# Kernel tuning notes

Measured on AMD Instinct MI355X. Metric: run time of the kernel, lower is better.

The kernel has to match this reference:

```python
import jax, jax.numpy as jnp
import numpy as np

B_BLK = 64      # sparse_block_size
LOCAL = 4       # sparse_local_num_blocks
GLOB = 2        # sparse_global_num_blocks
STRIDE = 4      # sparse_global_block_stride
NH = 16
NKV = 4
HD = 128
SCALE = HD ** -0.5
NEG = -1e9


def _build_block_index(num_blocks):
    """Static per-query-block key-block index table + validity mask."""
    max_sel = LOCAL + 1 + GLOB
    idx = np.zeros((num_blocks, max_sel), np.int32)
    valid = np.zeros((num_blocks, max_sel), bool)
    for t in range(num_blocks):
        local = list(range(max(0, t - LOCAL), t + 1))
        cand = list(range(0, t + 1, max(1, STRIDE)))
        glob = cand[-GLOB:] if (GLOB > 0 and len(cand) > 0) else []
        sel = sorted(set(local + glob))
        idx[t, :len(sel)] = sel
        valid[t, :len(sel)] = True
    return idx, valid


def _rotate_half(x):
    x1, x2 = jnp.split(x, 2, axis=-1)
    return jnp.concatenate((-x2, x1), axis=-1)


def setup_inputs() -> dict:
    key = jax.random.key(0)
    ks = jax.random.split(key, 7)
    bsz, S, H = 1, 4096, 2048
    return {
        "hidden_states": jax.random.normal(ks[0], (bsz, S, H), jnp.float32) * 0.02,
        "cos": jax.random.uniform(ks[1], (bsz, S, HD), jnp.float32, -1.0, 1.0),
        "sin": jax.random.uniform(ks[2], (bsz, S, HD), jnp.float32, -1.0, 1.0),
        "wq": jax.random.normal(ks[3], (NH * HD, H), jnp.float32) * 0.02,
        "wk": jax.random.normal(ks[4], (NKV * HD, H), jnp.float32) * 0.02,
        "wv": jax.random.normal(ks[5], (NKV * HD, H), jnp.float32) * 0.02,
        "wo": jax.random.normal(ks[6], (H, NH * HD), jnp.float32) * 0.02,
    }


def reference(hidden_states, cos, sin, wq, wk, wv, wo):
    b, S, H = hidden_states.shape
    # QKV projections (nn.Linear: x @ W.T), split heads -> [b, h, S, d]
    q = (hidden_states @ wq.T).reshape(b, S, NH, HD).transpose(0, 2, 1, 3)
    k = (hidden_states @ wk.T).reshape(b, S, NKV, HD).transpose(0, 2, 1, 3)
    v = (hidden_states @ wv.T).reshape(b, S, NKV, HD).transpose(0, 2, 1, 3)
    # RoPE (cos/sin broadcast over heads)
    c = cos[:, None, :, :]
    s = sin[:, None, :, :]
    q = q * c + _rotate_half(q) * s
    k = k * c + _rotate_half(k) * s
    # GQA: repeat KV heads
    n_rep = NH // NKV
    k = jnp.repeat(k, n_rep, axis=1)
    v = jnp.repeat(v, n_rep, axis=1)
    # Block-sparse local+global attention (S divisible by B_BLK -> no padding)
    T = S // B_BLK
    q_blk = q.reshape(b, NH, T, B_BLK, HD)
    k_blk = k.reshape(b, NH, T, B_BLK, HD)
    v_blk = v.reshape(b, NH, T, B_BLK, HD)
    idx, valid = _build_block_index(T)           # [T, Smax] static
    Smax = idx.shape[1]
    k_sel = k_blk[:, :, idx]                     # [b,h,T,Smax,Bk,d]
    v_sel = v_blk[:, :, idx]
    scores = jnp.einsum('bhtqd,bhtspd->bhtqsp', q_blk, k_sel) * SCALE
    # causal intra-block mask on the diagonal block, -inf on padded slots
    intra = jnp.triu(jnp.full((B_BLK, B_BLK), NEG, jnp.float32), 1)
    is_diag = jnp.asarray(idx == np.arange(T)[:, None], jnp.float32)  # [T,Smax]
    mask = is_diag[:, None, :, None] * intra[None, :, None, :]        # [T,Bq,Smax,Bk]
    mask = mask + jnp.where(jnp.asarray(valid)[:, None, :, None], 0.0, NEG)
    scores = scores + mask[None, None]
    scores = scores.reshape(b, NH, T, B_BLK, Smax * B_BLK)
    probs = jax.nn.softmax(scores, axis=-1)
    out = jnp.einsum('bhtqk,bhtkd->bhtqd', probs,
                     v_sel.reshape(b, NH, T, Smax * B_BLK, HD))
    out = out.reshape(b, NH, S, HD).transpose(0, 2, 1, 3).reshape(b, S, NH * HD)
    return out @ wo.T
```

## Files before the change

### kernel.cpp

```cpp
#include <hip/hip_runtime.h>

typedef unsigned short u16;
typedef short bf16x8 __attribute__((ext_vector_type(8)));
typedef float f32x4 __attribute__((ext_vector_type(4)));

#define S_LEN 4096
#define NHEADS 16
#define NKVH 4
#define HDIM 128
#define HID 2048
#define NQKV 3072

__device__ __forceinline__ u16 f2bf(float x) {
  union { float f; unsigned u; } v; v.f = x;
  unsigned r = v.u + 0x7fffu + ((v.u >> 16) & 1u);
  return (u16)(r >> 16);
}
__device__ __forceinline__ float bf2f(u16 x) {
  union { unsigned u; float f; } v; v.u = ((unsigned)x) << 16;
  return v.f;
}
__device__ __forceinline__ void async16(u16* lds, const u16* g) {
  __builtin_amdgcn_global_load_lds((const __attribute__((address_space(1))) void*)g,
                                   (__attribute__((address_space(3))) void*)lds, 16, 0, 0);
}

__global__ __launch_bounds__(256) void cast_f32_bf16(const float* __restrict__ in,
                                                     u16* __restrict__ out, int n4) {
  int i = blockIdx.x * 256 + threadIdx.x;
  if (i >= n4) return;
  float4 v = ((const float4*)in)[i];
  ushort4 o;
  o.x = f2bf(v.x); o.y = f2bf(v.y); o.z = f2bf(v.z); o.w = f2bf(v.w);
  ((ushort4*)out)[i] = o;
}

#define VMC4 asm volatile("s_waitcnt vmcnt(4)" ::: "memory")
#define VMC0 asm volatile("s_waitcnt vmcnt(0)" ::: "memory")
#define NOVM ((void)0)

#define STAGE_A(buf, h, kt) do { \
    async16(&As[buf][adst[h][0]], asrc[h][0] + (size_t)(kt) * 64); \
    async16(&As[buf][adst[h][1]], asrc[h][1] + (size_t)(kt) * 64); \
  } while (0)
#define STAGE_B(buf, h, kt) do { \
    async16(&Bs[buf][bdst[h][0]], bsrc[h][0] + (size_t)(kt) * 64); \
    async16(&Bs[buf][bdst[h][1]], bsrc[h][1] + (size_t)(kt) * 64); \
  } while (0)

#define RD_A(cur, mh) do { \
    _Pragma("unroll") \
    for (int i_ = 0; i_ < 4; ++i_) { \
      const int m64_ = (wm * 128 + ((mh) * 4 + i_) * 16 + l16) * 64; \
      af[i_][0] = *(const bf16x8*)&As[cur][m64_ + ((quad ^ x7) * 8)]; \
      af[i_][1] = *(const bf16x8*)&As[cur][m64_ + (((4 + quad) ^ x7) * 8)]; \
    } } while (0)

#define RD_B(cur, nh, dst) do { \
    _Pragma("unroll") \
    for (int j_ = 0; j_ < 2; ++j_) { \
      const int n64_ = (wn * 64 + ((nh) * 2 + j_) * 16 + l16) * 64; \
      dst[j_][0] = *(const bf16x8*)&Bs[cur][n64_ + ((quad ^ x7) * 8)]; \
      dst[j_][1] = *(const bf16x8*)&Bs[cur][n64_ + (((4 + quad) ^ x7) * 8)]; \
    } } while (0)

#define PH(READS, STAGE_STMT, MH, NH, BSET, VM) do { \
    READS; \
    STAGE_STMT; \
    __builtin_amdgcn_s_barrier(); \
    asm volatile("s_waitcnt lgkmcnt(0)" ::: "memory"); \
    __builtin_amdgcn_sched_barrier(0); \
    __builtin_amdgcn_s_setprio(1); \
    _Pragma("unroll") \
    for (int ks_ = 0; ks_ < 2; ++ks_) \
      _Pragma("unroll") \
      for (int i_ = 0; i_ < 4; ++i_) \
        _Pragma("unroll") \
        for (int j_ = 0; j_ < 2; ++j_) \
          acc[(MH) * 4 + i_][(NH) * 2 + j_] = __builtin_amdgcn_mfma_f32_16x16x32_bf16( \
              af[i_][ks_], BSET[j_][ks_], acc[(MH) * 4 + i_][(NH) * 2 + j_], 0, 0, 0); \
    __builtin_amdgcn_s_setprio(0); \
    VM; \
    __builtin_amdgcn_s_barrier(); \
  } while (0)

template<bool OUT_BF16>
__global__ __launch_bounds__(512, 2) void gemm8p(const u16* __restrict__ A, const u16* __restrict__ B,
                                                 void* __restrict__ Cp, int M, int N, int K) {
  __shared__ __align__(16) u16 As[2][256 * 64];
  __shared__ __align__(16) u16 Bs[2][256 * 64];
  const int tid = threadIdx.x;
  const int w = tid >> 6, l = tid & 63, quad = l >> 4, l16 = l & 15;
  const int wm = w >> 2, wn = w & 3;
  const int x7 = l16 & 7;
  const int bm = blockIdx.x, bn = blockIdx.y;

  const u16* asrc[2][2]; int adst[2][2];
  const u16* bsrc[2][2]; int bdst[2][2];
#pragma unroll
  for (int h = 0; h < 2; ++h)
#pragma unroll
    for (int j = 0; j < 2; ++j) {
      int u = j * 512 + w * 64 + l;
      int r = u >> 3, cc = u & 7;
      int ma = ((r >> 6) << 7) + (h << 6) + (r & 63);
      asrc[h][j] = A + (size_t)(bm * 256 + ma) * K + (size_t)((cc ^ (ma & 7)) * 8);
      int nb = ((r >> 5) << 6) + (h << 5) + (r & 31);
      bsrc[h][j] = B + (size_t)(bn * 256 + nb) * K + (size_t)((cc ^ (nb & 7)) * 8);
      int r0 = j * 64 + w * 8;
      adst[h][j] = (((r0 >> 6) << 7) + (h << 6) + (r0 & 63)) * 64;
      bdst[h][j] = (((r0 >> 5) << 6) + (h << 5) + (r0 & 31)) * 64;
    }

  f32x4 acc[8][4];
#pragma unroll
  for (int i = 0; i < 8; ++i)
#pragma unroll
    for (int j = 0; j < 4; ++j) acc[i][j] = f32x4{0.f, 0.f, 0.f, 0.f};

  bf16x8 af[4][2], b0f[2][2], b1f[2][2];

  STAGE_A(0, 0, 0); STAGE_B(0, 0, 0); STAGE_B(0, 1, 0); STAGE_A(0, 1, 0);
  STAGE_A(1, 0, 1); STAGE_B(1, 0, 1);
  VMC4;
  __builtin_amdgcn_s_barrier();

  const int NI = K >> 7;
  for (int it = 0; it < NI; ++it) {
    const int t1 = 2 * it + 1, t2 = 2 * it + 2, t3 = 2 * it + 3;
    const bool full = (it + 1 < NI);
    PH(RD_A(0, 0); RD_B(0, 0, b0f), STAGE_B(1, 1, t1),            0, 0, b0f, NOVM);
    PH(RD_B(0, 1, b1f),             STAGE_A(1, 1, t1),            0, 1, b1f, NOVM);
    PH(RD_A(0, 1),                  if (full) STAGE_A(0, 0, t2),  1, 1, b1f, NOVM);
    PH(((void)0),                   if (full) STAGE_B(0, 0, t2),  1, 0, b0f, if (full) VMC4; else VMC0);
    PH(RD_A(1, 0); RD_B(1, 0, b0f), if (full) STAGE_B(0, 1, t2),  0, 0, b0f, NOVM);
    PH(RD_B(1, 1, b1f),             if (full) STAGE_A(0, 1, t2),  0, 1, b1f, NOVM);
    PH(RD_A(1, 1),                  if (full) STAGE_A(1, 0, t3),  1, 1, b1f, NOVM);
    PH(((void)0),                   if (full) STAGE_B(1, 0, t3),  1, 0, b0f, if (full) VMC4);
  }

  const int row0 = bm * 256 + wm * 128;
  const int col0 = bn * 256 + wn * 64;
#pragma unroll
  for (int mf = 0; mf < 8; ++mf)
#pragma unroll
    for (int nf = 0; nf < 4; ++nf) {
      const int col = col0 + nf * 16 + l16;
#pragma unroll
      for (int r = 0; r < 4; ++r) {
        const int row = row0 + mf * 16 + quad * 4 + r;
        float v = acc[mf][nf][r];
        if (OUT_BF16) ((u16*)Cp)[(size_t)row * N + col] = f2bf(v);
        else          ((float*)Cp)[(size_t)row * N + col] = v;
      }
    }
}

__global__ __launch_bounds__(256) void rope_scatter(const u16* __restrict__ qkv,
                                                    const float* __restrict__ cosp,
                                                    const float* __restrict__ sinp,
                                                    u16* __restrict__ Q, u16* __restrict__ Kd) {
  int idx = blockIdx.x * 256 + threadIdx.x;
  int d = idx & 63;
  int hh = (idx >> 6) % 20;
  int s = idx / (20 * 64);
  size_t base = (size_t)s * NQKV + hh * 128;
  float x1 = bf2f(qkv[base + d]);
  float x2 = bf2f(qkv[base + d + 64]);
  float c1 = cosp[s * 128 + d], s1 = sinp[s * 128 + d];
  float c2 = cosp[s * 128 + d + 64], s2 = sinp[s * 128 + d + 64];
  float o1 = x1 * c1 - x2 * s1;
  float o2 = x2 * c2 + x1 * s2;
  u16* dst = (hh < NHEADS) ? (Q + ((size_t)hh * S_LEN + s) * HDIM)
                           : (Kd + ((size_t)(hh - NHEADS) * S_LEN + s) * HDIM);
  dst[d] = f2bf(o1);
  dst[d + 64] = f2bf(o2);
}

__global__ __launch_bounds__(256) void vtrans(const u16* __restrict__ qkv, u16* __restrict__ Vt) {
  __shared__ u16 tile[64][65];
  int s0 = blockIdx.x * 64;
  int j0 = blockIdx.y * 64;
  int tid = threadIdx.x;
  for (int it = 0; it < 16; ++it) {
    int lin = it * 256 + tid;
    int sr = lin >> 6, jc = lin & 63;
    tile[sr][jc] = qkv[(size_t)(s0 + sr) * NQKV + 2560 + j0 + jc];
  }
  __syncthreads();
  for (int it = 0; it < 16; ++it) {
    int lin = it * 256 + tid;
    int dr = lin >> 6, sc = lin & 63;
    Vt[(size_t)(j0 + dr) * S_LEN + s0 + sc] = tile[sc][dr];
  }
}

__global__ __launch_bounds__(256) void attn_kernel(const u16* __restrict__ Q, const u16* __restrict__ K,
                                                   const u16* __restrict__ Vt, u16* __restrict__ Aout) {
  const float SCALE = 0.08838834764831845f;
  const float NEGF = -3.0e38f;
  const int t = blockIdx.x, h = blockIdx.y;
  const int kvh = h >> 2;
  const int tid = threadIdx.x;
  const int w = tid >> 6, l = tid & 63, quad = l >> 4, l16 = l & 15;

  __shared__ __align__(16) u16 Qs[64 * 128];
  __shared__ __align__(16) u16 Ks[64 * 128];
  __shared__ __align__(16) u16 Vs[128 * 64];
  __shared__ __align__(16) u16 Ps[4 * 16 * 72];

  int sel[7]; int nsel = 0;
  {
    int g1 = (t >> 2) << 2, g0 = g1 - 4;
    int lo = t - 4; if (lo < 0) lo = 0;
    if (g0 >= 0 && g0 < lo) sel[nsel++] = g0;
    if (g1 < lo) sel[nsel++] = g1;
    for (int b = lo; b <= t; ++b) sel[nsel++] = b;
  }

  {
    const size_t qbase = ((size_t)h * S_LEN + t * 64) * HDIM;
    for (int j = 0; j < 4; ++j) {
      int slot = (w * 4 + j) * 64 + l;
      int m = slot >> 4;
      int c = (slot & 15) ^ (m & 15);
      async16(&Qs[(w * 4 + j) * 64 * 8], Q + qbase + m * 128 + c * 8);
    }
  }

  float m_run[4], l_run[4];
  for (int r = 0; r < 4; ++r) { m_run[r] = NEGF; l_run[r] = 0.f; }
  f32x4 oacc[8];
  for (int i = 0; i < 8; ++i) oacc[i] = f32x4{0.f, 0.f, 0.f, 0.f};

  for (int ib = 0; ib < nsel; ++ib) {
    const int kb = sel[ib];
    __syncthreads();
    {
      const size_t kbase = ((size_t)kvh * S_LEN + kb * 64) * HDIM;
      const size_t vbase = (size_t)kvh * HDIM * S_LEN + kb * 64;
      for (int j = 0; j < 4; ++j) {
        int slot = (w * 4 + j) * 64 + l;
        int mk = slot >> 4;
        int ck = (slot & 15) ^ (mk & 15);
        async16(&Ks[(w * 4 + j) * 64 * 8], K + kbase + mk * 128 + ck * 8);
        int dv = slot >> 3;
        int cv = (slot & 7) ^ (dv & 7);
        async16(&Vs[(w * 4 + j) * 64 * 8], Vt + vbase + (size_t)dv * S_LEN + cv * 8);
      }
    }
    __syncthreads();

    f32x4 sacc[4];
    for (int nt = 0; nt < 4; ++nt) sacc[nt] = f32x4{0.f, 0.f, 0.f, 0.f};
    const int mq = w * 16 + l16;
    for (int ks = 0; ks < 128; ks += 32) {
      int cb = (ks >> 3) + quad;
      bf16x8 af = *(const bf16x8*)&Qs[(mq * 16 + (cb ^ (mq & 15))) * 8];
      for (int nt = 0; nt < 4; ++nt) {
        int n = nt * 16 + l16;
        bf16x8 bv = *(const bf16x8*)&Ks[(n * 16 + (cb ^ (n & 15))) * 8];
        sacc[nt] = __builtin_amdgcn_mfma_f32_16x16x32_bf16(af, bv, sacc[nt], 0, 0, 0);
      }
    }

    const bool diag = (kb == t);
    float alpha[4];
    for (int r = 0; r < 4; ++r) {
      int qrow = w * 16 + quad * 4 + r;
      float pv[4];
      float vmax = NEGF;
      for (int nt = 0; nt < 4; ++nt) {
        float v = sacc[nt][r] * SCALE;
        if (diag && (nt * 16 + l16) > qrow) v = NEGF;
        pv[nt] = v;
        vmax = fmaxf(vmax, v);
      }
      for (int off = 1; off < 16; off <<= 1) vmax = fmaxf(vmax, __shfl_xor(vmax, off));
      float mnew = fmaxf(m_run[r], vmax);
      alpha[r] = __expf(m_run[r] - mnew);
      m_run[r] = mnew;
      float sum = 0.f;
      for (int nt = 0; nt < 4; ++nt) {
        float p = __expf(pv[nt] - mnew);
        sum += p;
        Ps[(w * 16 + quad * 4 + r) * 72 + nt * 16 + l16] = f2bf(p);
      }
      for (int off = 1; off < 16; off <<= 1) sum += __shfl_xor(sum, off);
      l_run[r] = l_run[r] * alpha[r] + sum;
    }
    for (int nt = 0; nt < 8; ++nt) {
      f32x4 o = oacc[nt];
      o[0] *= alpha[0]; o[1] *= alpha[1]; o[2] *= alpha[2]; o[3] *= alpha[3];
      oacc[nt] = o;
    }

    for (int ks = 0; ks < 64; ks += 32) {
      bf16x8 pf = *(const bf16x8*)&Ps[(w * 16 + l16) * 72 + ks + quad * 8];
      int cb = (ks >> 3) + quad;
      for (int nt = 0; nt < 8; ++nt) {
        int n = nt * 16 + l16;
        bf16x8 vv = *(const bf16x8*)&Vs[(n * 8 + (cb ^ (n & 7))) * 8];
        oacc[nt] = __builtin_amdgcn_mfma_f32_16x16x32_bf16(pf, vv, oacc[nt], 0, 0, 0);
      }
    }
  }

  float inv[4];
  for (int r = 0; r < 4; ++r) inv[r] = 1.f / l_run[r];
  const int srow = t * 64 + w * 16 + quad * 4;
  for (int nt = 0; nt < 8; ++nt) {
    int col = h * 128 + nt * 16 + l16;
    for (int r = 0; r < 4; ++r)
      Aout[(size_t)(srow + r) * HID + col] = f2bf(oacc[nt][r] * inv[r]);
  }
}

extern "C" void kernel_launch(void* const* d_in, const int* in_sizes, int n_in,
                              void* d_out, int out_size, void* d_ws, size_t ws_size,
                              hipStream_t stream) {
  const float* hs   = (const float*)d_in[0];
  const float* cosp = (const float*)d_in[1];
  const float* sinp = (const float*)d_in[2];
  const float* wq   = (const float*)d_in[3];
  const float* wk   = (const float*)d_in[4];
  const float* wv   = (const float*)d_in[5];
  const float* wo   = (const float*)d_in[6];

  u16* hsb = (u16*)d_ws;
  u16* W   = hsb + (size_t)S_LEN * HID;
  u16* wob = W + (size_t)NQKV * HID;
  u16* qkv = wob + (size_t)HID * HID;
  u16* Qm  = qkv + (size_t)S_LEN * NQKV;
  u16* Km  = Qm + (size_t)NHEADS * S_LEN * HDIM;
  u16* Vt  = Km + (size_t)NKVH * S_LEN * HDIM;
  u16* att = Vt + (size_t)NKVH * HDIM * S_LEN;

  cast_f32_bf16<<<8192, 256, 0, stream>>>(hs, hsb, 2097152);
  cast_f32_bf16<<<4096, 256, 0, stream>>>(wq, W, 1048576);
  cast_f32_bf16<<<1024, 256, 0, stream>>>(wk, W + (size_t)4194304, 262144);
  cast_f32_bf16<<<1024, 256, 0, stream>>>(wv, W + (size_t)5242880, 262144);
  cast_f32_bf16<<<4096, 256, 0, stream>>>(wo, wob, 1048576);

  gemm8p<true><<<dim3(16, 12), 512, 0, stream>>>(hsb, W, (void*)qkv, 4096, 3072, 2048);
  rope_scatter<<<20480, 256, 0, stream>>>(qkv, cosp, sinp, Qm, Km);
  vtrans<<<dim3(64, 8), 256, 0, stream>>>(qkv, Vt);
  attn_kernel<<<dim3(64, 16), 256, 0, stream>>>(Qm, Km, Vt, att);
  gemm8p<false><<<dim3(16, 8), 512, 0, stream>>>(att, wob, d_out, 4096, 2048, 2048);
}
```

Before: 310.8 us.

## Double-buffer LDS fragment reads to overlap ds_reads with MFMA in GEMM

Restructures the GEMM main loop so A and B register fragments are double-buffered. The next fragment's LDS reads are issued before the current MFMA block, with partial lgkmcnt waits instead of a full wait each phase. Global offsets become 32-bit unsigned with readfirstlane LDS destinations to cut address registers. Launch bounds drop to one block per SIMD pair, since the extra fragment registers likely exceed the two-block budget; this lowers occupancy and adds hazards from the hand-counted waits and reordered barriers.

```diff
diff --git a/kernel.cpp b/kernel.cpp
--- a/kernel.cpp
+++ b/kernel.cpp
@@ -37,26 +37,30 @@
 
 #define VMC4 asm volatile("s_waitcnt vmcnt(4)" ::: "memory")
 #define VMC0 asm volatile("s_waitcnt vmcnt(0)" ::: "memory")
-#define NOVM ((void)0)
+#define LGKM0  asm volatile("s_waitcnt lgkmcnt(0)" ::: "memory")
+#define LGKM4  asm volatile("s_waitcnt lgkmcnt(4)" ::: "memory")
+#define LGKM8  asm volatile("s_waitcnt lgkmcnt(8)" ::: "memory")
+#define LGKM12 asm volatile("s_waitcnt lgkmcnt(12)" ::: "memory")
+#define BAR __builtin_amdgcn_s_barrier()
 
 #define STAGE_A(buf, h, kt) do { \
-    async16(&As[buf][adst[h][0]], asrc[h][0] + (size_t)(kt) * 64); \
-    async16(&As[buf][adst[h][1]], asrc[h][1] + (size_t)(kt) * 64); \
+    async16(&As[buf][adst[h][0]], A + aoff[h][0] + (size_t)(kt) * 64); \
+    async16(&As[buf][adst[h][1]], A + aoff[h][1] + (size_t)(kt) * 64); \
   } while (0)
 #define STAGE_B(buf, h, kt) do { \
-    async16(&Bs[buf][bdst[h][0]], bsrc[h][0] + (size_t)(kt) * 64); \
-    async16(&Bs[buf][bdst[h][1]], bsrc[h][1] + (size_t)(kt) * 64); \
+    async16(&Bs[buf][bdst[h][0]], B + boff[h][0] + (size_t)(kt) * 64); \
+    async16(&Bs[buf][bdst[h][1]], B + boff[h][1] + (size_t)(kt) * 64); \
   } while (0)
 
-#define RD_A(cur, mh) do { \
+#define RD_A8(cur, mh, dst) do { \
     _Pragma("unroll") \
     for (int i_ = 0; i_ < 4; ++i_) { \
       const int m64_ = (wm * 128 + ((mh) * 4 + i_) * 16 + l16) * 64; \
-      af[i_][0] = *(const bf16x8*)&As[cur][m64_ + ((quad ^ x7) * 8)]; \
-      af[i_][1] = *(const bf16x8*)&As[cur][m64_ + (((4 + quad) ^ x7) * 8)]; \
+      dst[i_][0] = *(const bf16x8*)&As[cur][m64_ + ((quad ^ x7) * 8)]; \
+      dst[i_][1] = *(const bf16x8*)&As[cur][m64_ + (((4 + quad) ^ x7) * 8)]; \
     } } while (0)
 
-#define RD_B(cur, nh, dst) do { \
+#define RD_B4(cur, nh, dst) do { \
     _Pragma("unroll") \
     for (int j_ = 0; j_ < 2; ++j_) { \
       const int n64_ = (wn * 64 + ((nh) * 2 + j_) * 16 + l16) * 64; \
@@ -64,11 +68,7 @@
       dst[j_][1] = *(const bf16x8*)&Bs[cur][n64_ + (((4 + quad) ^ x7) * 8)]; \
     } } while (0)
 
-#define PH(READS, STAGE_STMT, MH, NH, BSET, VM) do { \
-    READS; \
-    STAGE_STMT; \
-    __builtin_amdgcn_s_barrier(); \
-    asm volatile("s_waitcnt lgkmcnt(0)" ::: "memory"); \
+#define MM(MH, NH, ASET, BSET) do { \
     __builtin_amdgcn_sched_barrier(0); \
     __builtin_amdgcn_s_setprio(1); \
     _Pragma("unroll") \
@@ -78,14 +78,12 @@
         _Pragma("unroll") \
         for (int j_ = 0; j_ < 2; ++j_) \
           acc[(MH) * 4 + i_][(NH) * 2 + j_] = __builtin_amdgcn_mfma_f32_16x16x32_bf16( \
-              af[i_][ks_], BSET[j_][ks_], acc[(MH) * 4 + i_][(NH) * 2 + j_], 0, 0, 0); \
+              ASET[i_][ks_], BSET[j_][ks_], acc[(MH) * 4 + i_][(NH) * 2 + j_], 0, 0, 0); \
     __builtin_amdgcn_s_setprio(0); \
-    VM; \
-    __builtin_amdgcn_s_barrier(); \
   } while (0)
 
 template<bool OUT_BF16>
-__global__ __launch_bounds__(512, 2) void gemm8p(const u16* __restrict__ A, const u16* __restrict__ B,
+__global__ __launch_bounds__(512, 1) void gemm8p(const u16* __restrict__ A, const u16* __restrict__ B,
                                                  void* __restrict__ Cp, int M, int N, int K) {
   __shared__ __align__(16) u16 As[2][256 * 64];
   __shared__ __align__(16) u16 Bs[2][256 * 64];
@@ -95,8 +93,8 @@
   const int x7 = l16 & 7;
   const int bm = blockIdx.x, bn = blockIdx.y;
 
-  const u16* asrc[2][2]; int adst[2][2];
-  const u16* bsrc[2][2]; int bdst[2][2];
+  unsigned aoff[2][2], boff[2][2];
+  int adst[2][2], bdst[2][2];
 #pragma unroll
   for (int h = 0; h < 2; ++h)
 #pragma unroll
@@ -104,12 +102,12 @@
       int u = j * 512 + w * 64 + l;
       int r = u >> 3, cc = u & 7;
       int ma = ((r >> 6) << 7) + (h << 6) + (r & 63);
-      asrc[h][j] = A + (size_t)(bm * 256 + ma) * K + (size_t)((cc ^ (ma & 7)) * 8);
+      aoff[h][j] = (unsigned)(bm * 256 + ma) * (unsigned)K + (unsigned)((cc ^ (ma & 7)) * 8);
       int nb = ((r >> 5) << 6) + (h << 5) + (r & 31);
-      bsrc[h][j] = B + (size_t)(bn * 256 + nb) * K + (size_t)((cc ^ (nb & 7)) * 8);
+      boff[h][j] = (unsigned)(bn * 256 + nb) * (unsigned)K + (unsigned)((cc ^ (nb & 7)) * 8);
       int r0 = j * 64 + w * 8;
-      adst[h][j] = (((r0 >> 6) << 7) + (h << 6) + (r0 & 63)) * 64;
-      bdst[h][j] = (((r0 >> 5) << 6) + (h << 5) + (r0 & 31)) * 64;
+      adst[h][j] = __builtin_amdgcn_readfirstlane((((r0 >> 6) << 7) + (h << 6) + (r0 & 63)) * 64);
+      bdst[h][j] = __builtin_amdgcn_readfirstlane((((r0 >> 5) << 6) + (h << 5) + (r0 & 31)) * 64);
     }
 
   f32x4 acc[8][4];
@@ -118,25 +116,38 @@
 #pragma unroll
     for (int j = 0; j < 4; ++j) acc[i][j] = f32x4{0.f, 0.f, 0.f, 0.f};
 
-  bf16x8 af[4][2], b0f[2][2], b1f[2][2];
+  bf16x8 aR0[4][2], aR1[4][2], bR0[2][2], bR1[2][2];
 
   STAGE_A(0, 0, 0); STAGE_B(0, 0, 0); STAGE_B(0, 1, 0); STAGE_A(0, 1, 0);
   STAGE_A(1, 0, 1); STAGE_B(1, 0, 1);
   VMC4;
-  __builtin_amdgcn_s_barrier();
+  BAR;
+  RD_A8(0, 0, aR0); RD_B4(0, 0, bR0);
 
   const int NI = K >> 7;
   for (int it = 0; it < NI; ++it) {
     const int t1 = 2 * it + 1, t2 = 2 * it + 2, t3 = 2 * it + 3;
     const bool full = (it + 1 < NI);
-    PH(RD_A(0, 0); RD_B(0, 0, b0f), STAGE_B(1, 1, t1),            0, 0, b0f, NOVM);
-    PH(RD_B(0, 1, b1f),             STAGE_A(1, 1, t1),            0, 1, b1f, NOVM);
-    PH(RD_A(0, 1),                  if (full) STAGE_A(0, 0, t2),  1, 1, b1f, NOVM);
-    PH(((void)0),                   if (full) STAGE_B(0, 0, t2),  1, 0, b0f, if (full) VMC4; else VMC0);
-    PH(RD_A(1, 0); RD_B(1, 0, b0f), if (full) STAGE_B(0, 1, t2),  0, 0, b0f, NOVM);
-    PH(RD_B(1, 1, b1f),             if (full) STAGE_A(0, 1, t2),  0, 1, b1f, NOVM);
-    PH(RD_A(1, 1),                  if (full) STAGE_A(1, 0, t3),  1, 1, b1f, NOVM);
-    PH(((void)0),                   if (full) STAGE_B(1, 0, t3),  1, 0, b0f, if (full) VMC4);
+    RD_A8(0, 1, aR1); STAGE_B(1, 1, t1);
+    BAR; LGKM8;  MM(0, 0, aR0, bR0);
+    RD_B4(0, 1, bR1); STAGE_A(1, 1, t1);
+    BAR; LGKM4;  MM(1, 0, aR1, bR0);
+    if (full) STAGE_A(0, 0, t2);
+    BAR; LGKM0;  MM(1, 1, aR1, bR1);
+    if (full) { STAGE_B(0, 0, t2); VMC4; } else VMC0;
+    BAR;
+    RD_A8(1, 0, aR1); RD_B4(1, 0, bR0);
+    LGKM12; MM(0, 1, aR0, bR1);
+    RD_A8(1, 1, aR0); if (full) STAGE_B(0, 1, t2);
+    BAR; LGKM8;  MM(0, 0, aR1, bR0);
+    RD_B4(1, 1, bR1); if (full) STAGE_A(0, 1, t2);
+    BAR; LGKM4;  MM(1, 0, aR0, bR0);
+    if (full) STAGE_A(1, 0, t3);
+    BAR; LGKM0;  MM(1, 1, aR0, bR1);
+    if (full) { STAGE_B(1, 0, t3); VMC4; }
+    BAR;
+    if (full) { RD_A8(0, 0, aR0); RD_B4(0, 0, bR0); LGKM12; MM(0, 1, aR1, bR1); }
+    else      { LGKM0; MM(0, 1, aR1, bR1); }
   }
 
   const int row0 = bm * 256 + wm * 128;
```

Result: slower. 484.0 us (+55.7%).
